# Kernel tuning notes

Hardware: AMD Instinct MI355X
Metric: run time of the kernel (lower is better)

The kernel has to match this reference:

```python
import jax, jax.numpy as jnp
import numpy as np

B = 32
L = 256
NUM_AA = 20
LAMBDA_SINGLE = 1.0
LAMBDA_PAIR = 0.2 * (L - 1)


def setup_inputs() -> dict:
    key = jax.random.key(0)
    k1, k2, k3 = jax.random.split(key, 3)
    x = jax.random.randint(k1, (B, L), 0, NUM_AA, dtype=jnp.int32)
    # Embedding(num, 1) init: normal(0, embedding_dim**-0.5) = std 1.0
    w_single = jax.random.normal(k2, (L * NUM_AA, 1), dtype=jnp.float32)
    w_pair = jax.random.normal(k3, (L * L * NUM_AA * NUM_AA, 1), dtype=jnp.float32)
    return {"x": x, "w_single": w_single, "w_pair": w_pair}


def reference(x, w_single, w_pair):
    ws = w_single[:, 0]  # [L*20]
    wp = w_pair[:, 0]    # [L*L*400]
    Bn, Ln = x.shape
    pos = jnp.arange(Ln, dtype=jnp.int32)

    # singles[b, i] = ws[i*20 + x[b, i]]
    singles = ws[pos[None, :] * NUM_AA + x]  # [B, L]
    all_singles = jnp.broadcast_to(ws.reshape(Ln, NUM_AA), (Bn, Ln, NUM_AA))  # [B, L, 20]

    # pairs[b, i, j] = wp[(i*L + j)*400 + x[b,i]*20 + x[b,j]]
    idx_pairs = (pos[:, None] * Ln + pos[None, :]) * (NUM_AA * NUM_AA) \
        + x[:, :, None] * NUM_AA + x[:, None, :]  # [B, L, L]
    pairs = wp[idx_pairs]  # [B, L, L]

    # all_pairs reproduces the original in-place mutation semantics:
    # at outer iteration i (inner loop over j), x[:, p] has already been
    # overwritten to 19 for p < i, equals j for p == i, and is original for p > i.
    i_ax = pos[None, :, None, None]                      # [1, L, 1, 1]
    p_ax = pos[None, None, :, None]                      # [1, 1, L, 1]
    j_ax = jnp.arange(NUM_AA, dtype=jnp.int32)[None, None, None, :]  # [1,1,1,20]
    x_b = x[:, None, :, None]                            # [B, 1, L, 1]
    eff = jnp.where(p_ax < i_ax, NUM_AA - 1, jnp.where(p_ax == i_ax, j_ax, x_b))
    idx_all = (i_ax * Ln + p_ax) * (NUM_AA * NUM_AA) + j_ax * NUM_AA + eff  # [B,L,L,20]
    all_pairs = wp[idx_all]  # [B, L, L, 20]

    energy = singles + jnp.sum(pairs, axis=2)  # [B, L]
    logits = all_singles + jnp.sum(all_pairs, axis=2)  # [B, L, 20]
    total_energy = jax.nn.logsumexp(logits, axis=-1)  # [B, L]
    final_energy = jnp.mean(jnp.sum(-energy + total_energy, axis=1))

    single_reg = LAMBDA_SINGLE * jnp.sum(jnp.square(w_single))
    pair_reg = LAMBDA_PAIR * jnp.sum(jnp.square(w_pair))
    single_lasso = LAMBDA_SINGLE * jnp.sum(jnp.abs(w_single))
    pair_lasso = LAMBDA_PAIR * jnp.sum(jnp.abs(w_pair))
    return final_energy + single_reg + pair_reg + single_lasso + pair_lasso
```

## Files before the change

kernel.cpp:

```cpp
#include <hip/hip_runtime.h>
#include <cmath>

#define Bsz 32
#define Lsz 256
#define Asz 20
#define NCHUNK 8
#define PCH 32
#define GRP 16
#define NGRP 2
#define BLK1 640

#define OFF_G 0
#define OFF_C (NCHUNK*Lsz*Bsz*Asz)
#define OFF_E (OFF_C + NCHUNK*Lsz*Asz)
#define OFF_RSQ (OFF_E + NCHUNK*Lsz*Bsz)
#define OFF_RAB (OFF_RSQ + NCHUNK*Lsz)
#define OFF_K2  (OFF_RAB + NCHUNK*Lsz)

__global__ __launch_bounds__(BLK1, 8) void k1(const int* __restrict__ x,
                                              const float* __restrict__ wp,
                                              float* __restrict__ ws) {
  const int wg = blockIdx.x;
  const int c = wg & (NCHUNK - 1);
  const int i = wg >> 3;
  const int t = threadIdx.x;
  const int j = t >> 5;
  const int b = t & 31;

  __shared__ float blk[GRP * 400];
  __shared__ int   xs[PCH * Bsz];
  __shared__ int   xi[Bsz];
  __shared__ float wred[32];

  const int pbase = c * PCH;
  for (int k = t; k < PCH * Bsz; k += BLK1) {
    int dp = k >> 5, bb = k & 31;
    xs[k] = x[bb * Lsz + pbase + dp];
  }
  if (t < Bsz) xi[t] = x[t * Lsz + i];

  float accJ = 0.f, accE = 0.f, accC = 0.f, rsq = 0.f, rab = 0.f;

  const float4* wrow = (const float4*)(wp + (size_t)(i * Lsz + pbase) * 400);
  float4 v0 = wrow[t];
  float4 v1 = wrow[t + 640];
  float4 v2 = (t < 320) ? wrow[t + 1280] : make_float4(0.f, 0.f, 0.f, 0.f);

  for (int g = 0; g < NGRP; ++g) {
    float4* bf4 = (float4*)blk;
    bf4[t] = v0;
    bf4[t + 640] = v1;
    if (t < 320) bf4[t + 1280] = v2;
    rsq += v0.x*v0.x + v0.y*v0.y + v0.z*v0.z + v0.w*v0.w;
    rsq += v1.x*v1.x + v1.y*v1.y + v1.z*v1.z + v1.w*v1.w;
    rab += fabsf(v0.x)+fabsf(v0.y)+fabsf(v0.z)+fabsf(v0.w);
    rab += fabsf(v1.x)+fabsf(v1.y)+fabsf(v1.z)+fabsf(v1.w);
    if (t < 320) {
      rsq += v2.x*v2.x + v2.y*v2.y + v2.z*v2.z + v2.w*v2.w;
      rab += fabsf(v2.x)+fabsf(v2.y)+fabsf(v2.z)+fabsf(v2.w);
    }
    __syncthreads();

    if (g == 0) {
      v0 = wrow[1600 + t];
      v1 = wrow[1600 + t + 640];
      if (t < 320) v2 = wrow[1600 + t + 1280];
    }

    const int p0 = pbase + g * GRP;
    int ppstart = i + 1 - p0;
    if (ppstart < 0) ppstart = 0;
    const int jbase = j * Asz;
    for (int pp = ppstart; pp < GRP; ++pp) {
      int xv = xs[((g * GRP + pp) << 5) | b];
      accJ += blk[pp * 400 + jbase + xv];
    }
    if (t < Bsz) {
      const int ebase = xi[t] * Asz;
      for (int pp = 0; pp < GRP; ++pp) {
        int xv = xs[((g * GRP + pp) << 5) | t];
        accE += blk[pp * 400 + ebase + xv];
      }
    } else if (t < Bsz + Asz) {
      const int jj = t - Bsz;
      int pend = i - p0;
      if (pend > GRP) pend = GRP;
      for (int pp = 0; pp < pend; ++pp) accC += blk[pp * 400 + jj * Asz + 19];
      const int pd = i - p0;
      if (pd >= 0 && pd < GRP) accC += blk[pd * 400 + jj * Asz + jj];
    }
    __syncthreads();
  }

  ws[OFF_G + ((size_t)(c * Lsz + i) * Bsz + b) * Asz + j] = accJ;
  if (t < Bsz) ws[OFF_E + (c * Lsz + i) * Bsz + t] = accE;
  else if (t < Bsz + Asz) ws[OFF_C + (c * Lsz + i) * Asz + (t - Bsz)] = accC;

  for (int s = 32; s >= 1; s >>= 1) {
    rsq += __shfl_down(rsq, s);
    rab += __shfl_down(rab, s);
  }
  if ((t & 63) == 0) { wred[t >> 6] = rsq; wred[16 + (t >> 6)] = rab; }
  __syncthreads();
  if (t == 0) {
    float a = 0.f, bb = 0.f;
    for (int w = 0; w < 10; ++w) { a += wred[w]; bb += wred[16 + w]; }
    ws[OFF_RSQ + wg] = a;
    ws[OFF_RAB + wg] = bb;
  }
}

__global__ __launch_bounds__(BLK1) void k2(const int* __restrict__ x,
                                           const float* __restrict__ wsng,
                                           const float* __restrict__ ws,
                                           float* __restrict__ wso) {
  const int i = blockIdx.x;
  const int t = threadIdx.x;
  const int j = t >> 5, b = t & 31;
  __shared__ float l[Bsz * 21];

  float v = wsng[i * Asz + j];
  #pragma unroll
  for (int c = 0; c < NCHUNK; ++c) {
    v += ws[OFF_C + (c * Lsz + i) * Asz + j];
    v += ws[OFF_G + ((size_t)(c * Lsz + i) * Bsz + b) * Asz + j];
  }
  l[b * 21 + j] = v;
  __syncthreads();

  if (t < Bsz) {
    float m = -1e30f;
    #pragma unroll
    for (int jj = 0; jj < Asz; ++jj) m = fmaxf(m, l[t * 21 + jj]);
    float se = 0.f;
    #pragma unroll
    for (int jj = 0; jj < Asz; ++jj) se += __expf(l[t * 21 + jj] - m);
    float lse = m + __logf(se);
    float en = wsng[i * Asz + x[t * Lsz + i]];
    #pragma unroll
    for (int c = 0; c < NCHUNK; ++c) en += ws[OFF_E + (c * Lsz + i) * Bsz + t];
    wso[OFF_K2 + i * Bsz + t] = lse - en;
  }
}

__global__ __launch_bounds__(256) void k3(const float* __restrict__ wsng,
                                          const float* __restrict__ ws,
                                          float* __restrict__ out) {
  const int t = threadIdx.x;
  float ssq = 0.f, sab = 0.f;
  for (int k = t; k < Lsz * Asz; k += 256) {
    float v = wsng[k];
    ssq += v * v; sab += fabsf(v);
  }
  float psq = 0.f, pab = 0.f;
  for (int k = t; k < NCHUNK * Lsz; k += 256) {
    psq += ws[OFF_RSQ + k];
    pab += ws[OFF_RAB + k];
  }
  float fe = 0.f;
  for (int k = t; k < Lsz * Bsz; k += 256) fe += ws[OFF_K2 + k];

  const float LP = 51.0f;
  float val = fe * (1.0f / Bsz) + (ssq + sab) + LP * (psq + pab);

  __shared__ float red[256];
  red[t] = val;
  __syncthreads();
  for (int s = 128; s >= 1; s >>= 1) {
    if (t < s) red[t] += red[t + s];
    __syncthreads();
  }
  if (t == 0) out[0] = red[0];
}

extern "C" void kernel_launch(void* const* d_in, const int* in_sizes, int n_in,
                              void* d_out, int out_size, void* d_ws, size_t ws_size,
                              hipStream_t stream) {
  const int*   x       = (const int*)d_in[0];
  const float* wsingle = (const float*)d_in[1];
  const float* wpair   = (const float*)d_in[2];
  float* ws  = (float*)d_ws;
  float* out = (float*)d_out;

  k1<<<Lsz * NCHUNK, BLK1, 0, stream>>>(x, wpair, ws);
  k2<<<Lsz, BLK1, 0, stream>>>(x, wsingle, ws, ws);
  k3<<<1, 256, 0, stream>>>(wsingle, ws, out);
}
```

Measured before the change: 178.2 us.

## Double-buffer pair-weight tiles via async global-to-LDS loads with fewer, longer workgroups

The pair-weight stream is restructured so each workgroup handles half a row (128 positions) instead of a 32-position chunk. The kernel stages 16-position tiles into two LDS buffers with global_load_lds, so the next tile's load overlaps compute on the current one. This amortises the per-workgroup x staging and partial-sum writeback across more work and shrinks the intermediate buffers k2 reads. In exchange there are fewer workgroups (512), more LDS per block and a lower occupancy hint, which may limit latency hiding on an HBM-bound stream.

```diff
diff --git a/kernel.cpp b/kernel.cpp
--- a/kernel.cpp
+++ b/kernel.cpp
@@ -4,109 +4,129 @@
 #define Bsz 32
 #define Lsz 256
 #define Asz 20
-#define NCHUNK 8
-#define PCH 32
-#define GRP 16
-#define NGRP 2
+
+#define NHALF 2
+#define HALF 128
+#define SUBB 16
+#define NST (HALF / SUBB)
+#define STF (SUBB * 400)
 #define BLK1 640
+#define NWG1 (Lsz * NHALF)
 
 #define OFF_G 0
-#define OFF_C (NCHUNK*Lsz*Bsz*Asz)
-#define OFF_E (OFF_C + NCHUNK*Lsz*Asz)
-#define OFF_RSQ (OFF_E + NCHUNK*Lsz*Bsz)
-#define OFF_RAB (OFF_RSQ + NCHUNK*Lsz)
-#define OFF_K2  (OFF_RAB + NCHUNK*Lsz)
-
-__global__ __launch_bounds__(BLK1, 8) void k1(const int* __restrict__ x,
+#define OFF_C (NHALF * Lsz * Bsz * Asz)
+#define OFF_E (OFF_C + NHALF * Lsz * Asz)
+#define OFF_RSQ (OFF_E + NHALF * Lsz * Bsz)
+#define OFF_RAB (OFF_RSQ + NWG1)
+#define OFF_K2  (OFF_RAB + NWG1)
+
+__device__ __forceinline__ void cp16(const float* g, float* l) {
+  __builtin_amdgcn_global_load_lds(
+      (const __attribute__((address_space(1))) void*)g,
+      (__attribute__((address_space(3))) void*)l, 16, 0, 0);
+}
+
+__global__ __launch_bounds__(BLK1, 5) void k1(const int* __restrict__ x,
                                               const float* __restrict__ wp,
                                               float* __restrict__ ws) {
   const int wg = blockIdx.x;
-  const int c = wg & (NCHUNK - 1);
-  const int i = wg >> 3;
+  const int i = wg >> 1;
+  const int h = wg & 1;
+  const int pbase = h * HALF;
   const int t = threadIdx.x;
   const int j = t >> 5;
   const int b = t & 31;
 
-  __shared__ float blk[GRP * 400];
-  __shared__ int   xs[PCH * Bsz];
+  __shared__ float buf[2][STF];
+  __shared__ int   xs[HALF * Bsz];
   __shared__ int   xi[Bsz];
   __shared__ float wred[32];
 
-  const int pbase = c * PCH;
-  for (int k = t; k < PCH * Bsz; k += BLK1) {
+  const float* wrow = wp + (size_t)(i * Lsz + pbase) * 400;
+  const int wbase = (t >> 6) << 8;
+
+  {
+    const float* g = wrow;
+    cp16(g + t * 4, &buf[0][wbase]);
+    cp16(g + 2560 + t * 4, &buf[0][2560 + wbase]);
+    if (t < 320) cp16(g + 5120 + t * 4, &buf[0][5120 + wbase]);
+  }
+  for (int k = t; k < HALF * Bsz; k += BLK1) {
     int dp = k >> 5, bb = k & 31;
     xs[k] = x[bb * Lsz + pbase + dp];
   }
   if (t < Bsz) xi[t] = x[t * Lsz + i];
+  __syncthreads();
 
   float accJ = 0.f, accE = 0.f, accC = 0.f, rsq = 0.f, rab = 0.f;
-
-  const float4* wrow = (const float4*)(wp + (size_t)(i * Lsz + pbase) * 400);
-  float4 v0 = wrow[t];
-  float4 v1 = wrow[t + 640];
-  float4 v2 = (t < 320) ? wrow[t + 1280] : make_float4(0.f, 0.f, 0.f, 0.f);
-
-  for (int g = 0; g < NGRP; ++g) {
-    float4* bf4 = (float4*)blk;
-    bf4[t] = v0;
-    bf4[t + 640] = v1;
-    if (t < 320) bf4[t + 1280] = v2;
-    rsq += v0.x*v0.x + v0.y*v0.y + v0.z*v0.z + v0.w*v0.w;
-    rsq += v1.x*v1.x + v1.y*v1.y + v1.z*v1.z + v1.w*v1.w;
-    rab += fabsf(v0.x)+fabsf(v0.y)+fabsf(v0.z)+fabsf(v0.w);
-    rab += fabsf(v1.x)+fabsf(v1.y)+fabsf(v1.z)+fabsf(v1.w);
-    if (t < 320) {
-      rsq += v2.x*v2.x + v2.y*v2.y + v2.z*v2.z + v2.w*v2.w;
-      rab += fabsf(v2.x)+fabsf(v2.y)+fabsf(v2.z)+fabsf(v2.w);
-    }
-    __syncthreads();
-
-    if (g == 0) {
-      v0 = wrow[1600 + t];
-      v1 = wrow[1600 + t + 640];
-      if (t < 320) v2 = wrow[1600 + t + 1280];
-    }
-
-    const int p0 = pbase + g * GRP;
-    int ppstart = i + 1 - p0;
+  const int jbase = j * Asz;
+
+  for (int s = 0; s < NST; ++s) {
+    const float* blk = buf[s & 1];
+
+    if (s + 1 < NST) {
+      const float* g = wrow + (size_t)(s + 1) * STF;
+      float* l = buf[(s + 1) & 1];
+      cp16(g + t * 4, l + wbase);
+      cp16(g + 2560 + t * 4, l + 2560 + wbase);
+      if (t < 320) cp16(g + 5120 + t * 4, l + 5120 + wbase);
+    }
+
+    const int sp = s * SUBB;
+    const int pg = pbase + sp;
+
+    int ppstart = i + 1 - pg;
     if (ppstart < 0) ppstart = 0;
-    const int jbase = j * Asz;
-    for (int pp = ppstart; pp < GRP; ++pp) {
-      int xv = xs[((g * GRP + pp) << 5) | b];
+    for (int pp = ppstart; pp < SUBB; ++pp) {
+      int xv = xs[((sp + pp) << 5) | b];
       accJ += blk[pp * 400 + jbase + xv];
     }
     if (t < Bsz) {
       const int ebase = xi[t] * Asz;
-      for (int pp = 0; pp < GRP; ++pp) {
-        int xv = xs[((g * GRP + pp) << 5) | t];
+      #pragma unroll
+      for (int pp = 0; pp < SUBB; ++pp) {
+        int xv = xs[((sp + pp) << 5) | t];
         accE += blk[pp * 400 + ebase + xv];
       }
     } else if (t < Bsz + Asz) {
       const int jj = t - Bsz;
-      int pend = i - p0;
-      if (pend > GRP) pend = GRP;
+      int pend = i - pg;
+      if (pend > SUBB) pend = SUBB;
       for (int pp = 0; pp < pend; ++pp) accC += blk[pp * 400 + jj * Asz + 19];
-      const int pd = i - p0;
-      if (pd >= 0 && pd < GRP) accC += blk[pd * 400 + jj * Asz + jj];
+      const int pd = i - pg;
+      if (pd >= 0 && pd < SUBB) accC += blk[pd * 400 + jj * Asz + jj];
+    }
+
+    const float4* bf4 = (const float4*)blk;
+    float4 v0 = bf4[t];
+    float4 v1 = bf4[t + 640];
+    rsq += v0.x*v0.x + v0.y*v0.y + v0.z*v0.z + v0.w*v0.w
+         + v1.x*v1.x + v1.y*v1.y + v1.z*v1.z + v1.w*v1.w;
+    rab += fabsf(v0.x)+fabsf(v0.y)+fabsf(v0.z)+fabsf(v0.w)
+         + fabsf(v1.x)+fabsf(v1.y)+fabsf(v1.z)+fabsf(v1.w);
+    if (t < 320) {
+      float4 v2 = bf4[t + 1280];
+      rsq += v2.x*v2.x + v2.y*v2.y + v2.z*v2.z + v2.w*v2.w;
+      rab += fabsf(v2.x)+fabsf(v2.y)+fabsf(v2.z)+fabsf(v2.w);
     }
     __syncthreads();
   }
 
-  ws[OFF_G + ((size_t)(c * Lsz + i) * Bsz + b) * Asz + j] = accJ;
-  if (t < Bsz) ws[OFF_E + (c * Lsz + i) * Bsz + t] = accE;
-  else if (t < Bsz + Asz) ws[OFF_C + (c * Lsz + i) * Asz + (t - Bsz)] = accC;
-
-  for (int s = 32; s >= 1; s >>= 1) {
-    rsq += __shfl_down(rsq, s);
-    rab += __shfl_down(rab, s);
+  ws[OFF_G + ((size_t)((h * Lsz + i) * Bsz + b)) * Asz + j] = accJ;
+  if (t < Bsz) ws[OFF_E + (h * Lsz + i) * Bsz + t] = accE;
+  else if (t < Bsz + Asz) ws[OFF_C + (h * Lsz + i) * Asz + (t - Bsz)] = accC;
+
+  for (int sft = 32; sft >= 1; sft >>= 1) {
+    rsq += __shfl_down(rsq, sft);
+    rab += __shfl_down(rab, sft);
   }
   if ((t & 63) == 0) { wred[t >> 6] = rsq; wred[16 + (t >> 6)] = rab; }
   __syncthreads();
   if (t == 0) {
-    float a = 0.f, bb = 0.f;
-    for (int w = 0; w < 10; ++w) { a += wred[w]; bb += wred[16 + w]; }
+    float a = 0.f, bb2 = 0.f;
+    for (int w = 0; w < BLK1 / 64; ++w) { a += wred[w]; bb2 += wred[16 + w]; }
     ws[OFF_RSQ + wg] = a;
-    ws[OFF_RAB + wg] = bb;
+    ws[OFF_RAB + wg] = bb2;
   }
 }
 
@@ -121,9 +141,9 @@
 
   float v = wsng[i * Asz + j];
   #pragma unroll
-  for (int c = 0; c < NCHUNK; ++c) {
-    v += ws[OFF_C + (c * Lsz + i) * Asz + j];
-    v += ws[OFF_G + ((size_t)(c * Lsz + i) * Bsz + b) * Asz + j];
+  for (int hh = 0; hh < NHALF; ++hh) {
+    v += ws[OFF_C + (hh * Lsz + i) * Asz + j];
+    v += ws[OFF_G + ((size_t)((hh * Lsz + i) * Bsz + b)) * Asz + j];
   }
   l[b * 21 + j] = v;
   __syncthreads();
@@ -138,7 +158,7 @@
     float lse = m + __logf(se);
     float en = wsng[i * Asz + x[t * Lsz + i]];
     #pragma unroll
-    for (int c = 0; c < NCHUNK; ++c) en += ws[OFF_E + (c * Lsz + i) * Bsz + t];
+    for (int hh = 0; hh < NHALF; ++hh) en += ws[OFF_E + (hh * Lsz + i) * Bsz + t];
     wso[OFF_K2 + i * Bsz + t] = lse - en;
   }
 }
@@ -153,7 +173,7 @@
     ssq += v * v; sab += fabsf(v);
   }
   float psq = 0.f, pab = 0.f;
-  for (int k = t; k < NCHUNK * Lsz; k += 256) {
+  for (int k = t; k < NWG1; k += 256) {
     psq += ws[OFF_RSQ + k];
     pab += ws[OFF_RAB + k];
   }
@@ -182,7 +202,7 @@
   float* ws  = (float*)d_ws;
   float* out = (float*)d_out;
 
-  k1<<<Lsz * NCHUNK, BLK1, 0, stream>>>(x, wpair, ws);
+  k1<<<NWG1, BLK1, 0, stream>>>(x, wpair, ws);
   k2<<<Lsz, BLK1, 0, stream>>>(x, wsingle, ws, ws);
   k3<<<1, 256, 0, stream>>>(wsingle, ws, out);
 }
```

New measurement: 185.8 us. 4.3% more time.
